# Optimization experiments

Measured on AMD Instinct MI355X. Metric: run time of the kernel, lower is better.

## Reference

```python
import jax, jax.numpy as jnp
import numpy as np

N_LEVELS = 16
N_FEATS = 2
LOG2_T = 19
BASE_RES = 16.0
FINEST_RES = 512.0
N_POINTS = 1048576

_PRIMES = jnp.array([1, 2654435761, 805459861], dtype=jnp.uint32)
_OFFSETS = jnp.array([[i, j, k] for i in (0, 1) for j in (0, 1) for k in (0, 1)], dtype=jnp.int32)  # [8,3]
_MASK = jnp.uint32(2 ** LOG2_T - 1)


def setup_inputs() -> dict:
    key = jax.random.key(0)
    k1, k2 = jax.random.split(key)
    x = jax.random.uniform(k1, (N_POINTS, 3), dtype=jnp.float32)
    # nn.init.uniform_(w, a=-1e-4, b=1e-4) per level; stacked [L, T, F]
    embeddings = jax.random.uniform(k2, (N_LEVELS, 2 ** LOG2_T, N_FEATS),
                                    dtype=jnp.float32, minval=-1e-4, maxval=1e-4)
    bounding_box = jnp.stack([jnp.zeros(3, jnp.float32), jnp.ones(3, jnp.float32)])  # [2,3]
    return {"x": x, "embeddings": embeddings, "bounding_box": bounding_box}


def _resolutions():
    b = np.exp((np.log(FINEST_RES) - np.log(BASE_RES)) / (N_LEVELS - 1))
    return jnp.asarray(np.floor(BASE_RES * b ** np.arange(N_LEVELS)), dtype=jnp.float32)  # [L]


def reference(x, embeddings, bounding_box):
    box_min, box_max = bounding_box[0], bounding_box[1]
    keep_mask = jnp.all((x >= box_min) & (x <= box_max), axis=-1)  # [N]
    xc = jnp.clip(x, box_min, box_max)  # clamped coords used for voxel indexing

    def level(emb, res):
        grid = (box_max - box_min) / res                              # [3]
        bl = jnp.floor((xc - box_min) / grid).astype(jnp.int32)       # [N,3] bottom-left voxel idx
        vmin = bl.astype(x.dtype) * grid + box_min                    # [N,3]
        w = (x - vmin) / grid                                         # [N,3] (original x, as in source)
        corners = bl[:, None, :] + _OFFSETS[None]                     # [N,8,3]
        h = corners.astype(jnp.uint32) * _PRIMES                      # wrap-around uint32 mul
        hashed = ((h[..., 0] ^ h[..., 1] ^ h[..., 2]) & _MASK).astype(jnp.int32)  # [N,8]
        v = emb[hashed]                                               # [N,8,F] gather
        wx, wy, wz = w[:, 0:1], w[:, 1:2], w[:, 2:3]
        c00 = v[:, 0] * (1 - wx) + v[:, 4] * wx
        c01 = v[:, 1] * (1 - wx) + v[:, 5] * wx
        c10 = v[:, 2] * (1 - wx) + v[:, 6] * wx
        c11 = v[:, 3] * (1 - wx) + v[:, 7] * wx
        c0 = c00 * (1 - wy) + c10 * wy
        c1 = c01 * (1 - wy) + c11 * wy
        return c0 * (1 - wz) + c1 * wz                                # [N,F]

    feats = jax.vmap(level)(embeddings, _resolutions())               # [L,N,F]
    out = jnp.transpose(feats, (1, 0, 2)).reshape(x.shape[0], N_LEVELS * N_FEATS)  # level-major concat
    return out, keep_mask
```

## Files before the change

kernel.cpp:

```cpp
#include <hip/hip_runtime.h>
#include <math.h>
#include <stdint.h>


#define NLEVELS 16
#define HASH_MASK 0x7FFFFu
#define TABLE_ENTRIES 524288

struct ResTable { float r[NLEVELS]; };

__device__ __forceinline__ float2 gather_one_level(
    const float* __restrict__ x, const float2* __restrict__ tbl,
    float bmin0, float bmin1, float bmin2,
    float bmax0, float bmax1, float bmax2,
    float res, int point)
{
    const float* xp = x + (size_t)point * 3;
    float x0 = xp[0], x1 = xp[1], x2 = xp[2];

    float xc0 = fminf(fmaxf(x0, bmin0), bmax0);
    float xc1 = fminf(fmaxf(x1, bmin1), bmax1);
    float xc2 = fminf(fmaxf(x2, bmin2), bmax2);

    float g0 = (bmax0 - bmin0) / res;
    float g1 = (bmax1 - bmin1) / res;
    float g2 = (bmax2 - bmin2) / res;

    float f0 = floorf((xc0 - bmin0) / g0);
    float f1 = floorf((xc1 - bmin1) / g1);
    float f2 = floorf((xc2 - bmin2) / g2);
    int b0 = (int)f0, b1 = (int)f1, b2 = (int)f2;

    float vmin0 = f0 * g0 + bmin0;
    float vmin1 = f1 * g1 + bmin1;
    float vmin2 = f2 * g2 + bmin2;
    float wx = (x0 - vmin0) / g0;
    float wy = (x1 - vmin1) / g1;
    float wz = (x2 - vmin2) / g2;

    uint32_t hx0 = (uint32_t)b0;
    uint32_t hx1 = (uint32_t)(b0 + 1);
    uint32_t hy0 = (uint32_t)b1 * 2654435761u;
    uint32_t hy1 = (uint32_t)(b1 + 1) * 2654435761u;
    uint32_t hz0 = (uint32_t)b2 * 805459861u;
    uint32_t hz1 = (uint32_t)(b2 + 1) * 805459861u;

    float2 v0 = tbl[(hx0 ^ hy0 ^ hz0) & HASH_MASK];
    float2 v1 = tbl[(hx0 ^ hy0 ^ hz1) & HASH_MASK];
    float2 v2 = tbl[(hx0 ^ hy1 ^ hz0) & HASH_MASK];
    float2 v3 = tbl[(hx0 ^ hy1 ^ hz1) & HASH_MASK];
    float2 v4 = tbl[(hx1 ^ hy0 ^ hz0) & HASH_MASK];
    float2 v5 = tbl[(hx1 ^ hy0 ^ hz1) & HASH_MASK];
    float2 v6 = tbl[(hx1 ^ hy1 ^ hz0) & HASH_MASK];
    float2 v7 = tbl[(hx1 ^ hy1 ^ hz1) & HASH_MASK];

    float omx = 1.0f - wx, omy = 1.0f - wy, omz = 1.0f - wz;

    float c00_0 = v0.x * omx + v4.x * wx;
    float c00_1 = v0.y * omx + v4.y * wx;
    float c01_0 = v1.x * omx + v5.x * wx;
    float c01_1 = v1.y * omx + v5.y * wx;
    float c10_0 = v2.x * omx + v6.x * wx;
    float c10_1 = v2.y * omx + v6.y * wx;
    float c11_0 = v3.x * omx + v7.x * wx;
    float c11_1 = v3.y * omx + v7.y * wx;

    float c0_0 = c00_0 * omy + c10_0 * wy;
    float c0_1 = c00_1 * omy + c10_1 * wy;
    float c1_0 = c01_0 * omy + c11_0 * wy;
    float c1_1 = c01_1 * omy + c11_1 * wy;

    float2 o;
    o.x = c0_0 * omz + c1_0 * wz;
    o.y = c0_1 * omz + c1_1 * wz;
    return o;
}

__global__ __launch_bounds__(256) void gather_level_kernel(
    const float* __restrict__ x,
    const float* __restrict__ emb,
    const float* __restrict__ bbox,
    float2* __restrict__ tmp,
    int n_points, int level_base, ResTable rt)
{
    int level = (blockIdx.x & 7) + level_base;
    int point = (blockIdx.x >> 3) * 256 + threadIdx.x;
    if (point >= n_points) return;

    float bmin0 = bbox[0], bmin1 = bbox[1], bmin2 = bbox[2];
    float bmax0 = bbox[3], bmax1 = bbox[4], bmax2 = bbox[5];

    const float2* tbl = (const float2*)emb + (size_t)level * TABLE_ENTRIES;
    float2 o = gather_one_level(x, tbl, bmin0, bmin1, bmin2,
                                bmax0, bmax1, bmax2, rt.r[level], point);
    tmp[(size_t)level * n_points + point] = o;
}

__global__ __launch_bounds__(256) void assemble_kernel(
    const float* __restrict__ x,
    const float2* __restrict__ tmp,
    const float* __restrict__ bbox,
    float* __restrict__ out,
    float* __restrict__ mask,
    int n_points)
{
    int p = blockIdx.x * 256 + threadIdx.x;
    if (p >= n_points) return;

    float4 o[8];
    float2* op = (float2*)o;
#pragma unroll
    for (int l = 0; l < NLEVELS; ++l)
        op[l] = tmp[(size_t)l * n_points + p];

    float4* dst = (float4*)(out + (size_t)p * 32);
#pragma unroll
    for (int j = 0; j < 8; ++j) dst[j] = o[j];

    float bmin0 = bbox[0], bmin1 = bbox[1], bmin2 = bbox[2];
    float bmax0 = bbox[3], bmax1 = bbox[4], bmax2 = bbox[5];
    const float* xp = x + (size_t)p * 3;
    float x0 = xp[0], x1 = xp[1], x2 = xp[2];
    bool keep = (x0 >= bmin0) & (x0 <= bmax0) &
                (x1 >= bmin1) & (x1 <= bmax1) &
                (x2 >= bmin2) & (x2 <= bmax2);
    mask[p] = keep ? 1.0f : 0.0f;
}

__global__ __launch_bounds__(256) void hash_embed_direct_kernel(
    const float* __restrict__ x,
    const float* __restrict__ emb,
    const float* __restrict__ bbox,
    float* __restrict__ out,
    float* __restrict__ mask,
    int n_points, ResTable rt)
{
    int tid = blockIdx.x * 256 + threadIdx.x;
    int point = tid >> 4;
    int level = tid & 15;
    if (point >= n_points) return;

    float bmin0 = bbox[0], bmin1 = bbox[1], bmin2 = bbox[2];
    float bmax0 = bbox[3], bmax1 = bbox[4], bmax2 = bbox[5];

    if (level == 0) {
        const float* xp = x + (size_t)point * 3;
        float x0 = xp[0], x1 = xp[1], x2 = xp[2];
        bool keep = (x0 >= bmin0) & (x0 <= bmax0) &
                    (x1 >= bmin1) & (x1 <= bmax1) &
                    (x2 >= bmin2) & (x2 <= bmax2);
        mask[point] = keep ? 1.0f : 0.0f;
    }

    const float2* tbl = (const float2*)emb + (size_t)level * TABLE_ENTRIES;
    float2 o = gather_one_level(x, tbl, bmin0, bmin1, bmin2,
                                bmax0, bmax1, bmax2, rt.r[level], point);
    *(float2*)(out + (size_t)point * 32 + level * 2) = o;
}

extern "C" void kernel_launch(void* const* d_in, const int* in_sizes, int n_in,
                              void* d_out, int out_size, void* d_ws, size_t ws_size,
                              hipStream_t stream) {
    const float* x    = (const float*)d_in[0];
    const float* emb  = (const float*)d_in[1];
    const float* bbox = (const float*)d_in[2];
    int n_points = in_sizes[0] / 3;

    float* out  = (float*)d_out;
    float* mask = out + (size_t)n_points * 32;

    ResTable rt;
    double b = exp((log(512.0) - log(16.0)) / 15.0);
    for (int l = 0; l < NLEVELS; ++l)
        rt.r[l] = (float)floor(16.0 * pow(b, (double)l));

    size_t tmp_bytes = (size_t)n_points * NLEVELS * sizeof(float2);
    if (ws_size >= tmp_bytes) {
        float2* tmp = (float2*)d_ws;
        int chunks = (n_points + 255) / 256;
        dim3 grid(chunks * 8);
        hipLaunchKernelGGL(gather_level_kernel, grid, dim3(256), 0, stream,
                           x, emb, bbox, tmp, n_points, 0, rt);
        hipLaunchKernelGGL(gather_level_kernel, grid, dim3(256), 0, stream,
                           x, emb, bbox, tmp, n_points, 8, rt);
        hipLaunchKernelGGL(assemble_kernel, dim3(chunks), dim3(256), 0, stream,
                           x, tmp, bbox, out, mask, n_points);
    } else {
        long long total = (long long)n_points * NLEVELS;
        int blocks = (int)((total + 255) / 256);
        hipLaunchKernelGGL(hash_embed_direct_kernel, dim3(blocks), dim3(256), 0,
                           stream, x, emb, bbox, out, mask, n_points, rt);
    }
}
```

Measured before the change: 603.0 us.

## Fuse all levels into one kernel with LDS-staged coalesced output writes

```diff
diff --git a/kernel.cpp b/kernel.cpp
--- a/kernel.cpp
+++ b/kernel.cpp
@@ -9,19 +9,14 @@
 
 struct ResTable { float r[NLEVELS]; };
 
-__device__ __forceinline__ float2 gather_one_level(
-    const float* __restrict__ x, const float2* __restrict__ tbl,
+__device__ __forceinline__ float2 level_gather(
+    float x0, float x1, float x2,
+    float xc0, float xc1, float xc2,
+    const float2* __restrict__ tbl,
     float bmin0, float bmin1, float bmin2,
     float bmax0, float bmax1, float bmax2,
-    float res, int point)
+    float res)
 {
-    const float* xp = x + (size_t)point * 3;
-    float x0 = xp[0], x1 = xp[1], x2 = xp[2];
-
-    float xc0 = fminf(fmaxf(x0, bmin0), bmax0);
-    float xc1 = fminf(fmaxf(x1, bmin1), bmax1);
-    float xc2 = fminf(fmaxf(x2, bmin2), bmax2);
-
     float g0 = (bmax0 - bmin0) / res;
     float g1 = (bmax1 - bmin1) / res;
     float g2 = (bmax2 - bmin2) / res;
@@ -76,58 +71,7 @@
     return o;
 }
 
-__global__ __launch_bounds__(256) void gather_level_kernel(
-    const float* __restrict__ x,
-    const float* __restrict__ emb,
-    const float* __restrict__ bbox,
-    float2* __restrict__ tmp,
-    int n_points, int level_base, ResTable rt)
-{
-    int level = (blockIdx.x & 7) + level_base;
-    int point = (blockIdx.x >> 3) * 256 + threadIdx.x;
-    if (point >= n_points) return;
-
-    float bmin0 = bbox[0], bmin1 = bbox[1], bmin2 = bbox[2];
-    float bmax0 = bbox[3], bmax1 = bbox[4], bmax2 = bbox[5];
-
-    const float2* tbl = (const float2*)emb + (size_t)level * TABLE_ENTRIES;
-    float2 o = gather_one_level(x, tbl, bmin0, bmin1, bmin2,
-                                bmax0, bmax1, bmax2, rt.r[level], point);
-    tmp[(size_t)level * n_points + point] = o;
-}
-
-__global__ __launch_bounds__(256) void assemble_kernel(
-    const float* __restrict__ x,
-    const float2* __restrict__ tmp,
-    const float* __restrict__ bbox,
-    float* __restrict__ out,
-    float* __restrict__ mask,
-    int n_points)
-{
-    int p = blockIdx.x * 256 + threadIdx.x;
-    if (p >= n_points) return;
-
-    float4 o[8];
-    float2* op = (float2*)o;
-#pragma unroll
-    for (int l = 0; l < NLEVELS; ++l)
-        op[l] = tmp[(size_t)l * n_points + p];
-
-    float4* dst = (float4*)(out + (size_t)p * 32);
-#pragma unroll
-    for (int j = 0; j < 8; ++j) dst[j] = o[j];
-
-    float bmin0 = bbox[0], bmin1 = bbox[1], bmin2 = bbox[2];
-    float bmax0 = bbox[3], bmax1 = bbox[4], bmax2 = bbox[5];
-    const float* xp = x + (size_t)p * 3;
-    float x0 = xp[0], x1 = xp[1], x2 = xp[2];
-    bool keep = (x0 >= bmin0) & (x0 <= bmax0) &
-                (x1 >= bmin1) & (x1 <= bmax1) &
-                (x2 >= bmin2) & (x2 <= bmax2);
-    mask[p] = keep ? 1.0f : 0.0f;
-}
-
-__global__ __launch_bounds__(256) void hash_embed_direct_kernel(
+__global__ __launch_bounds__(256, 4) void fused_hash_embed_kernel(
     const float* __restrict__ x,
     const float* __restrict__ emb,
     const float* __restrict__ bbox,
@@ -135,27 +79,56 @@
     float* __restrict__ mask,
     int n_points, ResTable rt)
 {
-    int tid = blockIdx.x * 256 + threadIdx.x;
-    int point = tid >> 4;
-    int level = tid & 15;
-    if (point >= n_points) return;
+    __shared__ float lds[256 * 33];
+
+    const int tid = threadIdx.x;
+    const int p0 = blockIdx.x * 256;
+    const int p = p0 + tid;
+    const bool active = (p < n_points);
 
     float bmin0 = bbox[0], bmin1 = bbox[1], bmin2 = bbox[2];
     float bmax0 = bbox[3], bmax1 = bbox[4], bmax2 = bbox[5];
 
-    if (level == 0) {
-        const float* xp = x + (size_t)point * 3;
-        float x0 = xp[0], x1 = xp[1], x2 = xp[2];
+    float x0 = bmin0, x1 = bmin1, x2 = bmin2;
+    if (active) {
+        const float* xp = x + (size_t)p * 3;
+        x0 = xp[0]; x1 = xp[1]; x2 = xp[2];
         bool keep = (x0 >= bmin0) & (x0 <= bmax0) &
                     (x1 >= bmin1) & (x1 <= bmax1) &
                     (x2 >= bmin2) & (x2 <= bmax2);
-        mask[point] = keep ? 1.0f : 0.0f;
+        mask[p] = keep ? 1.0f : 0.0f;
     }
 
-    const float2* tbl = (const float2*)emb + (size_t)level * TABLE_ENTRIES;
-    float2 o = gather_one_level(x, tbl, bmin0, bmin1, bmin2,
-                                bmax0, bmax1, bmax2, rt.r[level], point);
-    *(float2*)(out + (size_t)point * 32 + level * 2) = o;
+    float xc0 = fminf(fmaxf(x0, bmin0), bmax0);
+    float xc1 = fminf(fmaxf(x1, bmin1), bmax1);
+    float xc2 = fminf(fmaxf(x2, bmin2), bmax2);
+
+#pragma unroll
+    for (int l = 0; l < NLEVELS; ++l) {
+        const float2* tbl = (const float2*)emb + (size_t)l * TABLE_ENTRIES;
+        float2 o = level_gather(x0, x1, x2, xc0, xc1, xc2, tbl,
+                                bmin0, bmin1, bmin2,
+                                bmax0, bmax1, bmax2, rt.r[l]);
+        lds[tid * 33 + 2 * l]     = o.x;
+        lds[tid * 33 + 2 * l + 1] = o.y;
+    }
+
+    __syncthreads();
+
+    int nblk = n_points - p0;
+    if (nblk > 256) nblk = 256;
+    const int nfloat4 = nblk * 8;
+    float4* dst = (float4*)(out + (size_t)p0 * 32);
+#pragma unroll
+    for (int j = 0; j < 8; ++j) {
+        int v = j * 256 + tid;
+        if (v < nfloat4) {
+            int q = v >> 3;
+            int k = (v & 7) << 2;
+            const float* s = &lds[q * 33 + k];
+            dst[v] = make_float4(s[0], s[1], s[2], s[3]);
+        }
+    }
 }
 
 extern "C" void kernel_launch(void* const* d_in, const int* in_sizes, int n_in,
@@ -174,21 +147,7 @@
     for (int l = 0; l < NLEVELS; ++l)
         rt.r[l] = (float)floor(16.0 * pow(b, (double)l));
 
-    size_t tmp_bytes = (size_t)n_points * NLEVELS * sizeof(float2);
-    if (ws_size >= tmp_bytes) {
-        float2* tmp = (float2*)d_ws;
-        int chunks = (n_points + 255) / 256;
-        dim3 grid(chunks * 8);
-        hipLaunchKernelGGL(gather_level_kernel, grid, dim3(256), 0, stream,
-                           x, emb, bbox, tmp, n_points, 0, rt);
-        hipLaunchKernelGGL(gather_level_kernel, grid, dim3(256), 0, stream,
-                           x, emb, bbox, tmp, n_points, 8, rt);
-        hipLaunchKernelGGL(assemble_kernel, dim3(chunks), dim3(256), 0, stream,
-                           x, tmp, bbox, out, mask, n_points);
-    } else {
-        long long total = (long long)n_points * NLEVELS;
-        int blocks = (int)((total + 255) / 256);
-        hipLaunchKernelGGL(hash_embed_direct_kernel, dim3(blocks), dim3(256), 0,
-                           stream, x, emb, bbox, out, mask, n_points, rt);
-    }
+    int blocks = (n_points + 255) / 256;
+    hipLaunchKernelGGL(fused_hash_embed_kernel, dim3(blocks), dim3(256), 0,
+                       stream, x, emb, bbox, out, mask, n_points, rt);
 }
```

After: 794.4 us. +31.7%, slower.

## Precompute dense compact grids for coarse levels and coalesce output via LDS

Applied to the files above, without the earlier changes.

```diff
diff --git a/kernel.cpp b/kernel.cpp
--- a/kernel.cpp
+++ b/kernel.cpp
@@ -8,6 +8,7 @@
 #define TABLE_ENTRIES 524288
 
 struct ResTable { float r[NLEVELS]; };
+struct CompactMeta { int dim[8]; int off[8]; };
 
 __device__ __forceinline__ float2 gather_one_level(
     const float* __restrict__ x, const float2* __restrict__ tbl,
@@ -96,7 +97,109 @@
     tmp[(size_t)level * n_points + point] = o;
 }
 
-__global__ __launch_bounds__(256) void assemble_kernel(
+__global__ __launch_bounds__(256) void build_compact_kernel(
+    const float* __restrict__ emb,
+    float2* __restrict__ compact,
+    CompactMeta cm, int total)
+{
+    int id = blockIdx.x * 256 + threadIdx.x;
+    if (id >= total) return;
+
+    int l = 0;
+#pragma unroll
+    for (int t = 1; t < 8; ++t)
+        if (id >= cm.off[t]) l = t;
+    int local = id - cm.off[l];
+    int D = cm.dim[l];
+
+    int k = local % D;
+    int t2 = local / D;
+    int j = t2 % D;
+    int i = t2 / D;
+
+    uint32_t h = (uint32_t)i
+               ^ ((uint32_t)j * 2654435761u)
+               ^ ((uint32_t)k * 805459861u);
+    const float2* tbl = (const float2*)emb + (size_t)l * TABLE_ENTRIES;
+    compact[id] = tbl[h & HASH_MASK];
+}
+
+__global__ __launch_bounds__(256) void gather_compact_kernel(
+    const float* __restrict__ x,
+    const float2* __restrict__ compact,
+    const float* __restrict__ bbox,
+    float2* __restrict__ tmp,
+    int n_points, CompactMeta cm, ResTable rt)
+{
+    int level = blockIdx.x & 7;
+    int point = (blockIdx.x >> 3) * 256 + threadIdx.x;
+    if (point >= n_points) return;
+
+    float bmin0 = bbox[0], bmin1 = bbox[1], bmin2 = bbox[2];
+    float bmax0 = bbox[3], bmax1 = bbox[4], bmax2 = bbox[5];
+    float res = rt.r[level];
+
+    const float* xp = x + (size_t)point * 3;
+    float x0 = xp[0], x1 = xp[1], x2 = xp[2];
+
+    float xc0 = fminf(fmaxf(x0, bmin0), bmax0);
+    float xc1 = fminf(fmaxf(x1, bmin1), bmax1);
+    float xc2 = fminf(fmaxf(x2, bmin2), bmax2);
+
+    float g0 = (bmax0 - bmin0) / res;
+    float g1 = (bmax1 - bmin1) / res;
+    float g2 = (bmax2 - bmin2) / res;
+
+    float f0 = floorf((xc0 - bmin0) / g0);
+    float f1 = floorf((xc1 - bmin1) / g1);
+    float f2 = floorf((xc2 - bmin2) / g2);
+    int b0 = (int)f0, b1 = (int)f1, b2 = (int)f2;
+
+    float vmin0 = f0 * g0 + bmin0;
+    float vmin1 = f1 * g1 + bmin1;
+    float vmin2 = f2 * g2 + bmin2;
+    float wx = (x0 - vmin0) / g0;
+    float wy = (x1 - vmin1) / g1;
+    float wz = (x2 - vmin2) / g2;
+
+    int D = cm.dim[level];
+    const float2* tb = compact + cm.off[level];
+    int base = (b0 * D + b1) * D + b2;
+    int dj = D;
+    int di = D * D;
+
+    float2 v0 = tb[base];
+    float2 v1 = tb[base + 1];
+    float2 v2 = tb[base + dj];
+    float2 v3 = tb[base + dj + 1];
+    float2 v4 = tb[base + di];
+    float2 v5 = tb[base + di + 1];
+    float2 v6 = tb[base + di + dj];
+    float2 v7 = tb[base + di + dj + 1];
+
+    float omx = 1.0f - wx, omy = 1.0f - wy, omz = 1.0f - wz;
+
+    float c00_0 = v0.x * omx + v4.x * wx;
+    float c00_1 = v0.y * omx + v4.y * wx;
+    float c01_0 = v1.x * omx + v5.x * wx;
+    float c01_1 = v1.y * omx + v5.y * wx;
+    float c10_0 = v2.x * omx + v6.x * wx;
+    float c10_1 = v2.y * omx + v6.y * wx;
+    float c11_0 = v3.x * omx + v7.x * wx;
+    float c11_1 = v3.y * omx + v7.y * wx;
+
+    float c0_0 = c00_0 * omy + c10_0 * wy;
+    float c0_1 = c00_1 * omy + c10_1 * wy;
+    float c1_0 = c01_0 * omy + c11_0 * wy;
+    float c1_1 = c01_1 * omy + c11_1 * wy;
+
+    float2 o;
+    o.x = c0_0 * omz + c1_0 * wz;
+    o.y = c0_1 * omz + c1_1 * wz;
+    tmp[(size_t)level * n_points + point] = o;
+}
+
+__global__ __launch_bounds__(256) void assemble_lds_kernel(
     const float* __restrict__ x,
     const float2* __restrict__ tmp,
     const float* __restrict__ bbox,
@@ -104,27 +207,45 @@
     float* __restrict__ mask,
     int n_points)
 {
-    int p = blockIdx.x * 256 + threadIdx.x;
-    if (p >= n_points) return;
-
-    float4 o[8];
-    float2* op = (float2*)o;
+    __shared__ float lds[256 * 33];
+
+    const int tid = threadIdx.x;
+    const int p0 = blockIdx.x * 256;
+    const int p = p0 + tid;
+
+    if (p < n_points) {
 #pragma unroll
-    for (int l = 0; l < NLEVELS; ++l)
-        op[l] = tmp[(size_t)l * n_points + p];
-
-    float4* dst = (float4*)(out + (size_t)p * 32);
+        for (int l = 0; l < NLEVELS; ++l) {
+            float2 v = tmp[(size_t)l * n_points + p];
+            lds[tid * 33 + 2 * l]     = v.x;
+            lds[tid * 33 + 2 * l + 1] = v.y;
+        }
+        float bmin0 = bbox[0], bmin1 = bbox[1], bmin2 = bbox[2];
+        float bmax0 = bbox[3], bmax1 = bbox[4], bmax2 = bbox[5];
+        const float* xp = x + (size_t)p * 3;
+        float x0 = xp[0], x1 = xp[1], x2 = xp[2];
+        bool keep = (x0 >= bmin0) & (x0 <= bmax0) &
+                    (x1 >= bmin1) & (x1 <= bmax1) &
+                    (x2 >= bmin2) & (x2 <= bmax2);
+        mask[p] = keep ? 1.0f : 0.0f;
+    }
+
+    __syncthreads();
+
+    int nblk = n_points - p0;
+    if (nblk > 256) nblk = 256;
+    const int nfloat4 = nblk * 8;
+    float4* dst = (float4*)(out + (size_t)p0 * 32);
 #pragma unroll
-    for (int j = 0; j < 8; ++j) dst[j] = o[j];
-
-    float bmin0 = bbox[0], bmin1 = bbox[1], bmin2 = bbox[2];
-    float bmax0 = bbox[3], bmax1 = bbox[4], bmax2 = bbox[5];
-    const float* xp = x + (size_t)p * 3;
-    float x0 = xp[0], x1 = xp[1], x2 = xp[2];
-    bool keep = (x0 >= bmin0) & (x0 <= bmax0) &
-                (x1 >= bmin1) & (x1 <= bmax1) &
-                (x2 >= bmin2) & (x2 <= bmax2);
-    mask[p] = keep ? 1.0f : 0.0f;
+    for (int j = 0; j < 8; ++j) {
+        int v = j * 256 + tid;
+        if (v < nfloat4) {
+            int q = v >> 3;
+            int k = (v & 7) << 2;
+            const float* s = &lds[q * 33 + k];
+            dst[v] = make_float4(s[0], s[1], s[2], s[3]);
+        }
+    }
 }
 
 __global__ __launch_bounds__(256) void hash_embed_direct_kernel(
@@ -174,17 +295,44 @@
     for (int l = 0; l < NLEVELS; ++l)
         rt.r[l] = (float)floor(16.0 * pow(b, (double)l));
 
+    CompactMeta cm;
+    int total_compact = 0;
+    for (int l = 0; l < 8; ++l) {
+        int D = (int)rt.r[l] + 2;
+        cm.dim[l] = D;
+        cm.off[l] = total_compact;
+        total_compact += D * D * D;
+    }
     size_t tmp_bytes = (size_t)n_points * NLEVELS * sizeof(float2);
-    if (ws_size >= tmp_bytes) {
+    size_t compact_bytes = (size_t)total_compact * sizeof(float2);
+
+    int chunks = (n_points + 255) / 256;
+
+    if (ws_size >= tmp_bytes + compact_bytes) {
         float2* tmp = (float2*)d_ws;
-        int chunks = (n_points + 255) / 256;
+        float2* compact = (float2*)((char*)d_ws + tmp_bytes);
+
+        int pre_blocks = (total_compact + 255) / 256;
+        hipLaunchKernelGGL(build_compact_kernel, dim3(pre_blocks), dim3(256),
+                           0, stream, emb, compact, cm, total_compact);
+
+        dim3 grid(chunks * 8);
+        hipLaunchKernelGGL(gather_level_kernel, grid, dim3(256), 0, stream,
+                           x, emb, bbox, tmp, n_points, 8, rt);
+        hipLaunchKernelGGL(gather_compact_kernel, grid, dim3(256), 0, stream,
+                           x, compact, bbox, tmp, n_points, cm, rt);
+
+        hipLaunchKernelGGL(assemble_lds_kernel, dim3(chunks), dim3(256), 0,
+                           stream, x, tmp, bbox, out, mask, n_points);
+    } else if (ws_size >= tmp_bytes) {
+        float2* tmp = (float2*)d_ws;
         dim3 grid(chunks * 8);
         hipLaunchKernelGGL(gather_level_kernel, grid, dim3(256), 0, stream,
                            x, emb, bbox, tmp, n_points, 0, rt);
         hipLaunchKernelGGL(gather_level_kernel, grid, dim3(256), 0, stream,
                            x, emb, bbox, tmp, n_points, 8, rt);
-        hipLaunchKernelGGL(assemble_kernel, dim3(chunks), dim3(256), 0, stream,
-                           x, tmp, bbox, out, mask, n_points);
+        hipLaunchKernelGGL(assemble_lds_kernel, dim3(chunks), dim3(256), 0,
+                           stream, x, tmp, bbox, out, mask, n_points);
     } else {
         long long total = (long long)n_points * NLEVELS;
         int blocks = (int)((total + 255) / 256);
```

Result: no change. 593.3 us (-1.6%).
